# Performance work log

Hardware: AMD Instinct MI355X
Metric: run time of the kernel (lower is better)

## Reference

```python
import jax, jax.numpy as jnp
import numpy as np

H, P, N, D, T, MLPW, B = 64, 4, 16, 8, 64, 512, 2048
D_IN = 1 + H + P * H  # 321


def _linear_init(key, i, o):
    k1, k2 = jax.random.split(key)
    s = 1.0 / np.sqrt(i)
    W = jax.random.uniform(k1, (i, o), jnp.float32, -s, s)
    b = jax.random.uniform(k2, (o,), jnp.float32, -s, s)
    return W, b


def setup_inputs() -> dict:
    key = jax.random.key(0)
    ks = jax.random.split(key, 10)
    dims_f = [(D_IN, MLPW), (MLPW, MLPW), (MLPW, MLPW), (MLPW, H)]
    dims_g = [(D_IN, MLPW), (MLPW, MLPW), (MLPW, MLPW), (MLPW, H * N)]
    inp = {}
    for idx, (i, o) in enumerate(dims_f):
        W, b = _linear_init(ks[idx], i, o)
        inp[f"fW{idx}"], inp[f"fb{idx}"] = W, b
    for idx, (i, o) in enumerate(dims_g):
        W, b = _linear_init(ks[4 + idx], i, o)
        inp[f"gW{idx}"], inp[f"gb{idx}"] = W, b
    inp["rW"], inp["rb"] = _linear_init(ks[8], H, D)
    inp["ts"] = jnp.arange(T, dtype=jnp.float32)  # uniform grid, dt = 1
    inp["dbt"] = jax.random.normal(ks[9], (T - 1, B, N), jnp.float32)  # per-step randn noise
    inp["batch_size"] = B
    return inp


def _mlp(x, params):
    # Linear+ReLU stack, final Linear with tanh (tscale=1.0)
    for W, b in params[:-1]:
        x = jax.nn.relu(x @ W + b)
    W, b = params[-1]
    return jnp.tanh(x @ W + b)


def _forward(ts, dbt, fp, gp, rW, rb, batch_size):
    x0 = jnp.ones((batch_size, H), jnp.float32)  # fixed=True initial state
    dt = ts[1] - ts[0]  # dt_scale = 1
    hist = jnp.zeros((T, batch_size, H), jnp.float32).at[0].set(x0)
    curr_x, curr_t = x0, ts[0]
    xs = [x0]
    for k in range(T - 1):  # one integration step per output interval (uniform ts)
        # ortho rfft over the growing state history (length k+1); keep first P coeffs,
        # real part (matches torch complex -> .float() cast), zero-pad to P.
        coeffs = jnp.fft.rfft(hist[: k + 1], axis=0, norm="ortho")  # (F, B, H) complex
        c = jnp.real(coeffs[:P]).astype(jnp.float32)
        if c.shape[0] < P:
            c = jnp.concatenate(
                [c, jnp.zeros((P - c.shape[0], batch_size, H), jnp.float32)], axis=0
            )
        feats = jnp.transpose(c, (1, 0, 2)).reshape(batch_size, P * H)  # (B, P*H)
        tcol = jnp.broadcast_to(jnp.reshape(curr_t, (1, 1)), (batch_size, 1))
        tx = jnp.concatenate([tcol, curr_x, feats], axis=1)  # (B, 1+H+P*H)
        drift = _mlp(tx, fp)  # (B, H)
        diff = _mlp(tx, gp).reshape(batch_size, H, N)  # (B, H, N)
        curr_x = curr_x + drift * dt + jnp.einsum("bhn,bn->bh", diff, dbt[k])
        curr_t = jnp.minimum(curr_t + dt, ts[-1])
        hist = hist.at[k + 1].set(curr_x)
        xs.append(curr_x)  # linear_interp degenerates to curr_x on uniform grid
    xs = jnp.stack(xs, axis=1)  # (B, T, H)
    ys = xs @ rW + rb  # readout, (B, T, D)
    tse = jnp.broadcast_to(ts[None, :, None], (batch_size, T, 1))
    # linear_interpolation_coeffs is identity for NaN-free data
    return jnp.concatenate([tse, ys], axis=2)  # (B, T, 1+D)


def reference(fW0, fb0, fW1, fb1, fW2, fb2, fW3, fb3,
              gW0, gb0, gW1, gb1, gW2, gb2, gW3, gb3,
              rW, rb, ts, dbt, batch_size):
    fp = [(fW0, fb0), (fW1, fb1), (fW2, fb2), (fW3, fb3)]
    gp = [(gW0, gb0), (gW1, gb1), (gW2, gb2), (gW3, gb3)]
    return _forward(ts, dbt, fp, gp, rW, rb, batch_size)
```

## Files before the change

kernel.cpp:

```cpp
#include <hip/hip_runtime.h>
#include <math.h>

constexpr int kH   = 64;
constexpr int kP   = 4;
constexpr int kN   = 16;
constexpr int kD   = 8;
constexpr int kT   = 64;
constexpr int kWd  = 512;
constexpr int kB   = 2048;
constexpr int kDIN = 1 + kH + kP * kH;
constexpr int kKP  = 384;
constexpr int kBH  = kB * kH;

typedef __attribute__((ext_vector_type(8))) short short8;
typedef __attribute__((ext_vector_type(4))) float f32x4;

__device__ __forceinline__ short f2bf(float x) {
    union { float f; unsigned u; } v; v.f = x;
    unsigned r = (v.u + 0x7FFFu + ((v.u >> 16) & 1u)) >> 16;
    return (short)r;
}
__device__ __forceinline__ float bf2f(short h) {
    union { unsigned u; float f; } v; v.u = ((unsigned)(unsigned short)h) << 16;
    return v.f;
}

__device__ __forceinline__ void gload16(const short* g, short* l) {
    __builtin_amdgcn_global_load_lds(
        (const __attribute__((address_space(1))) unsigned int*)g,
        (__attribute__((address_space(3))) unsigned int*)l, 16, 0, 0);
}

__global__ __launch_bounds__(256) void transpose_bf16(const float* __restrict__ W,
                                                      short* __restrict__ Wt,
                                                      int K, int N, int Kp, int Np) {
    int idx = blockIdx.x * 256 + threadIdx.x;
    if (idx >= Kp * Np) return;
    int n = idx / Kp, kk = idx % Kp;
    float v = (kk < K && n < N) ? W[(size_t)kk * N + n] : 0.f;
    Wt[idx] = f2bf(v);
}

__global__ __launch_bounds__(256) void prep_bias(const float* __restrict__ fb0,
                                                 const float* __restrict__ gb0,
                                                 float* __restrict__ b0c) {
    int i = blockIdx.x * 256 + threadIdx.x;
    if (i < 1024) b0c[i] = (i < kWd) ? fb0[i] : gb0[i - kWd];
}

__global__ __launch_bounds__(256) void init_k(float* __restrict__ hist,
                                              short* __restrict__ txh) {
    int idx = blockIdx.x * 256 + threadIdx.x;
    if (idx < kBH) hist[idx] = 1.0f;
    if (idx < kB * (kKP - kDIN)) {
        int b = idx / (kKP - kDIN), c = idx % (kKP - kDIN);
        txh[(size_t)b * kKP + kDIN + c] = 0;
    }
}

__global__ __launch_bounds__(256) void step_pre(float* __restrict__ hist,
                                                const float* __restrict__ drift,
                                                const short* __restrict__ diffb,
                                                const float* __restrict__ dbt,
                                                short* __restrict__ txh, int k) {
    const int L = k + 1;
    __shared__ float ctab[kT * kP];
    int tid = threadIdx.x;
    float invs = rsqrtf((float)L);
    for (int i = tid; i < L * kP; i += 256) {
        int j = i >> 2, p = i & 3;
        ctab[i] = cosf(6.283185307179586f * (float)(p * j) / (float)L) * invs;
    }
    __syncthreads();
    int idx = blockIdx.x * 256 + tid;
    int b = idx >> 6, h = idx & 63;
    float xk;
    if (k == 0) {
        xk = 1.0f;
    } else {
        xk = hist[(size_t)(k - 1) * kBH + idx] + drift[idx];
        const short* dr = diffb + (size_t)b * 1024 + h * kN;
        const float* wr = dbt + (size_t)(k - 1) * kB * kN + b * kN;
#pragma unroll
        for (int n = 0; n < kN; ++n) xk += bf2f(dr[n]) * wr[n];
        hist[(size_t)k * kBH + idx] = xk;
    }
    const float* hp = hist + (size_t)b * kH + h;
    float a0 = 0.f, a1 = 0.f, a2 = 0.f, a3 = 0.f;
    for (int j = 0; j < k; ++j) {
        float x = hp[(size_t)j * kBH];
        a0 += x * ctab[j * 4 + 0];
        a1 += x * ctab[j * 4 + 1];
        a2 += x * ctab[j * 4 + 2];
        a3 += x * ctab[j * 4 + 3];
    }
    a0 += xk * ctab[k * 4 + 0];
    a1 += xk * ctab[k * 4 + 1];
    a2 += xk * ctab[k * 4 + 2];
    a3 += xk * ctab[k * 4 + 3];
    if (L < 2) a1 = 0.f;
    if (L < 4) a2 = 0.f;
    if (L < 6) a3 = 0.f;
    short* th = txh + (size_t)b * kKP;
    th[1 + kH + 0 * kH + h] = f2bf(a0);
    th[1 + kH + 1 * kH + h] = f2bf(a1);
    th[1 + kH + 2 * kH + h] = f2bf(a2);
    th[1 + kH + 3 * kH + h] = f2bf(a3);
    th[1 + h] = f2bf(xk);
    if (h == 0) th[0] = f2bf((float)k);
}

struct MArg {
    const short* A;
    const short* Bt;
    const float* bias;
    short* Cb;
    float* Cf;
    int K, lda, ldc, act, Nw;
};

__global__ __launch_bounds__(256, 2) void gemm_mfma(MArg f, MArg g, int ysplit) {
    const int y = blockIdx.y;
    MArg a;
    int n0;
    if (y < ysplit) { a = f; n0 = y * 64; }
    else            { a = g; n0 = (y - ysplit) * 64; }
    const int m0 = blockIdx.x * 64;

    __shared__ __align__(16) short sA[2][2][64 * 32];
    __shared__ __align__(16) short sB[2][2][64 * 32];

    const int tid = threadIdx.x;
    const int lane = tid & 63;
    const int w = tid >> 6;
    const int wm = (w & 1) * 32;
    const int wn = (w >> 1) * 32;

    const int sr = tid >> 2;
    const int s  = tid & 3;
    const int scol = (s ^ ((sr >> 1) & 3)) * 8;
    const int sdst = sr * 32 + s * 8;

    const short* gA = a.A  + (size_t)(m0 + sr) * a.lda + scol;
    const short* gB = a.Bt + (size_t)(n0 + sr) * a.K   + scol;

    const int nk = a.K >> 6;
    f32x4 acc[2][2] = {};

    gload16(gA,      &sA[0][0][sdst]);
    gload16(gA + 32, &sA[0][1][sdst]);
    gload16(gB,      &sB[0][0][sdst]);
    gload16(gB + 32, &sB[0][1][sdst]);

    const int fr = lane & 15;
    const int kb = ((lane >> 4) ^ ((fr >> 1) & 3)) * 8;
    const int ra0 = (wm + fr) * 32 + kb, ra1 = (wm + 16 + fr) * 32 + kb;
    const int rb0 = (wn + fr) * 32 + kb, rb1 = (wn + 16 + fr) * 32 + kb;

    for (int kt = 0; kt < nk; ++kt) {
        __syncthreads();
        const int cur = kt & 1, nxt = cur ^ 1;
        if (kt + 1 < nk) {
            const int ko = (kt + 1) << 6;
            gload16(gA + ko,      &sA[nxt][0][sdst]);
            gload16(gA + ko + 32, &sA[nxt][1][sdst]);
            gload16(gB + ko,      &sB[nxt][0][sdst]);
            gload16(gB + ko + 32, &sB[nxt][1][sdst]);
        }
#pragma unroll
        for (int ks = 0; ks < 2; ++ks) {
            short8 a0 = *(const short8*)&sA[cur][ks][ra0];
            short8 a1 = *(const short8*)&sA[cur][ks][ra1];
            short8 b0 = *(const short8*)&sB[cur][ks][rb0];
            short8 b1 = *(const short8*)&sB[cur][ks][rb1];
            acc[0][0] = __builtin_amdgcn_mfma_f32_16x16x32_bf16(a0, b0, acc[0][0], 0, 0, 0);
            acc[0][1] = __builtin_amdgcn_mfma_f32_16x16x32_bf16(a0, b1, acc[0][1], 0, 0, 0);
            acc[1][0] = __builtin_amdgcn_mfma_f32_16x16x32_bf16(a1, b0, acc[1][0], 0, 0, 0);
            acc[1][1] = __builtin_amdgcn_mfma_f32_16x16x32_bf16(a1, b1, acc[1][1], 0, 0, 0);
        }
    }

    const int rq = (lane >> 4) * 4;
#pragma unroll
    for (int j = 0; j < 2; ++j) {
        int n = n0 + wn + j * 16 + fr;
        if (n >= a.Nw) continue;
        float bias = a.bias[n];
#pragma unroll
        for (int i = 0; i < 2; ++i) {
#pragma unroll
            for (int r = 0; r < 4; ++r) {
                int m = m0 + wm + i * 16 + rq + r;
                float v = acc[i][j][r] + bias;
                if (a.act == 0) {
                    a.Cb[(size_t)m * a.ldc + n] = f2bf(fmaxf(v, 0.f));
                } else if (a.Cb) {
                    a.Cb[(size_t)m * a.ldc + n] = f2bf(tanhf(v));
                } else {
                    a.Cf[(size_t)m * a.ldc + n] = tanhf(v);
                }
            }
        }
    }
}

__global__ __launch_bounds__(256) void update_k(float* __restrict__ hist,
                                                const float* __restrict__ drift,
                                                const short* __restrict__ diffb,
                                                const float* __restrict__ dbt, int k) {
    int idx = blockIdx.x * 256 + threadIdx.x;
    int b = idx >> 6, h = idx & 63;
    float s = hist[(size_t)k * kBH + idx] + drift[idx];
    const short* dr = diffb + (size_t)b * 1024 + h * kN;
    const float* wr = dbt + (size_t)k * kB * kN + b * kN;
#pragma unroll
    for (int n = 0; n < kN; ++n) s += bf2f(dr[n]) * wr[n];
    hist[(size_t)(k + 1) * kBH + idx] = s;
}

__global__ __launch_bounds__(256) void readout_k(const float* __restrict__ hist,
                                                 const float* __restrict__ rW,
                                                 const float* __restrict__ rb,
                                                 const float* __restrict__ ts,
                                                 float* __restrict__ out) {
    __shared__ float sW[kH * kD];
    __shared__ float sb[kD];
    __shared__ float sts[kT];
    int tid = threadIdx.x;
    sW[tid] = rW[tid];
    sW[tid + 256] = rW[tid + 256];
    if (tid < kD) sb[tid] = rb[tid];
    if (tid < kT) sts[tid] = ts[tid];
    __syncthreads();
    int idx = blockIdx.x * 256 + tid;
    int t = idx & (kT - 1), b = idx >> 6;
    const float* xr = hist + (size_t)t * kBH + (size_t)b * kH;
    float acc[kD];
#pragma unroll
    for (int d = 0; d < kD; ++d) acc[d] = sb[d];
    for (int h = 0; h < kH; ++h) {
        float x = xr[h];
#pragma unroll
        for (int d = 0; d < kD; ++d) acc[d] += x * sW[h * kD + d];
    }
    float* o = out + (size_t)((size_t)b * kT + t) * (1 + kD);
    o[0] = sts[t];
#pragma unroll
    for (int d = 0; d < kD; ++d) o[1 + d] = acc[d];
}

extern "C" void kernel_launch(void* const* d_in, const int* in_sizes, int n_in,
                              void* d_out, int out_size, void* d_ws, size_t ws_size,
                              hipStream_t stream) {
    const float* fW0 = (const float*)d_in[0];  const float* fb0 = (const float*)d_in[1];
    const float* fW1 = (const float*)d_in[2];  const float* fb1 = (const float*)d_in[3];
    const float* fW2 = (const float*)d_in[4];  const float* fb2 = (const float*)d_in[5];
    const float* fW3 = (const float*)d_in[6];  const float* fb3 = (const float*)d_in[7];
    const float* gW0 = (const float*)d_in[8];  const float* gb0 = (const float*)d_in[9];
    const float* gW1 = (const float*)d_in[10]; const float* gb1 = (const float*)d_in[11];
    const float* gW2 = (const float*)d_in[12]; const float* gb2 = (const float*)d_in[13];
    const float* gW3 = (const float*)d_in[14]; const float* gb3 = (const float*)d_in[15];
    const float* rW  = (const float*)d_in[16]; const float* rb  = (const float*)d_in[17];
    const float* ts  = (const float*)d_in[18]; const float* dbt = (const float*)d_in[19];
    float* out = (float*)d_out;

    char* p = (char*)d_ws;
    float* hist  = (float*)p;  p += (size_t)kT * kBH * 4;
    float* drift = (float*)p;  p += (size_t)kBH * 4;
    float* b0c   = (float*)p;  p += 1024 * 4;
    short* diffb = (short*)p;  p += (size_t)kB * 1024 * 2;
    short* txh   = (short*)p;  p += (size_t)kB * kKP * 2;
    short* b1h   = (short*)p;  p += (size_t)kB * 1024 * 2;
    short* b2h   = (short*)p;  p += (size_t)kB * 1024 * 2;
    short* W0t   = (short*)p;  p += (size_t)1024 * kKP * 2;
    short* fW1t  = (short*)p;  p += (size_t)512 * 512 * 2;
    short* gW1t  = (short*)p;  p += (size_t)512 * 512 * 2;
    short* fW2t  = (short*)p;  p += (size_t)512 * 512 * 2;
    short* gW2t  = (short*)p;  p += (size_t)512 * 512 * 2;
    short* fW3t  = (short*)p;  p += (size_t)64 * 512 * 2;
    short* gW3t  = (short*)p;  p += (size_t)1024 * 512 * 2;

    auto tgrid = [](int n) { return dim3((n + 255) / 256); };
    transpose_bf16<<<tgrid(kKP * 512), 256, 0, stream>>>(fW0, W0t, kDIN, 512, kKP, 512);
    transpose_bf16<<<tgrid(kKP * 512), 256, 0, stream>>>(gW0, W0t + (size_t)512 * kKP, kDIN, 512, kKP, 512);
    transpose_bf16<<<tgrid(512 * 512), 256, 0, stream>>>(fW1, fW1t, 512, 512, 512, 512);
    transpose_bf16<<<tgrid(512 * 512), 256, 0, stream>>>(gW1, gW1t, 512, 512, 512, 512);
    transpose_bf16<<<tgrid(512 * 512), 256, 0, stream>>>(fW2, fW2t, 512, 512, 512, 512);
    transpose_bf16<<<tgrid(512 * 512), 256, 0, stream>>>(gW2, gW2t, 512, 512, 512, 512);
    transpose_bf16<<<tgrid(512 * 64), 256, 0, stream>>>(fW3, fW3t, 512, 64, 512, 64);
    transpose_bf16<<<tgrid(512 * 1024), 256, 0, stream>>>(gW3, gW3t, 512, 1024, 512, 1024);
    prep_bias<<<dim3(4), 256, 0, stream>>>(fb0, gb0, b0c);
    init_k<<<dim3(kBH / 256), 256, 0, stream>>>(hist, txh);

    for (int k = 0; k < kT - 1; ++k) {
        step_pre<<<dim3(kBH / 256), 256, 0, stream>>>(hist, drift, diffb, dbt, txh, k);

        MArg l1{txh, W0t, b0c, b1h, nullptr, kKP, kKP, 1024, 0, 1024};
        gemm_mfma<<<dim3(32, 16), 256, 0, stream>>>(l1, l1, 16);

        MArg f2{b1h, fW1t, fb1, b2h, nullptr, 512, 1024, 1024, 0, 512};
        MArg g2{b1h + 512, gW1t, gb1, b2h + 512, nullptr, 512, 1024, 1024, 0, 512};
        gemm_mfma<<<dim3(32, 16), 256, 0, stream>>>(f2, g2, 8);

        MArg f3{b2h, fW2t, fb2, b1h, nullptr, 512, 1024, 1024, 0, 512};
        MArg g3{b2h + 512, gW2t, gb2, b1h + 512, nullptr, 512, 1024, 1024, 0, 512};
        gemm_mfma<<<dim3(32, 16), 256, 0, stream>>>(f3, g3, 8);

        MArg f4{b1h, fW3t, fb3, nullptr, drift, 512, 1024, kH, 1, kH};
        MArg g4{b1h + 512, gW3t, gb3, diffb, nullptr, 512, 1024, 1024, 1, 1024};
        gemm_mfma<<<dim3(32, 17), 256, 0, stream>>>(f4, g4, 1);
    }

    update_k<<<dim3(kBH / 256), 256, 0, stream>>>(hist, drift, diffb, dbt, kT - 2);
    readout_k<<<dim3(kB * kT / 256), 256, 0, stream>>>(hist, rW, rb, ts, out);
}
```

Measured before the change: 2.548 ms.

## Fuse diffusion-noise contraction into last GEMM and enlarge GEMM tiles to 128 rows

The last MLP layer moves into a dedicated kernel. It applies tanh, multiplies the diffusion output by the Brownian increments staged in shared memory, and reduces over N with lane shuffles. It writes a per-(b,h) xdelta instead of a bf16 diffusion matrix, which removes the 2048x1024 intermediate write and reread and drops the bf16 rounding of diff. The general GEMM tiles grow from 64x64 with 256 threads to 128x64 with 512 threads, halving the block count and reusing each B tile across more rows. The larger tiles give fewer blocks (256) on a large-CU GPU, which may reduce occupancy.

Measured after the change: 2.608 ms. 2.4% more time.

```diff
diff --git a/kernel.cpp b/kernel.cpp
--- a/kernel.cpp
+++ b/kernel.cpp
@@ -14,15 +14,12 @@
 
 typedef __attribute__((ext_vector_type(8))) short short8;
 typedef __attribute__((ext_vector_type(4))) float f32x4;
+typedef __attribute__((ext_vector_type(4))) float float4v;
 
 __device__ __forceinline__ short f2bf(float x) {
     union { float f; unsigned u; } v; v.f = x;
     unsigned r = (v.u + 0x7FFFu + ((v.u >> 16) & 1u)) >> 16;
     return (short)r;
-}
-__device__ __forceinline__ float bf2f(short h) {
-    union { unsigned u; float f; } v; v.u = ((unsigned)(unsigned short)h) << 16;
-    return v.f;
 }
 
 __device__ __forceinline__ void gload16(const short* g, short* l) {
@@ -60,8 +57,7 @@
 
 __global__ __launch_bounds__(256) void step_pre(float* __restrict__ hist,
                                                 const float* __restrict__ drift,
-                                                const short* __restrict__ diffb,
-                                                const float* __restrict__ dbt,
+                                                const float* __restrict__ xdelta,
                                                 short* __restrict__ txh, int k) {
     const int L = k + 1;
     __shared__ float ctab[kT * kP];
@@ -78,11 +74,7 @@
     if (k == 0) {
         xk = 1.0f;
     } else {
-        xk = hist[(size_t)(k - 1) * kBH + idx] + drift[idx];
-        const short* dr = diffb + (size_t)b * 1024 + h * kN;
-        const float* wr = dbt + (size_t)(k - 1) * kB * kN + b * kN;
-#pragma unroll
-        for (int n = 0; n < kN; ++n) xk += bf2f(dr[n]) * wr[n];
+        xk = hist[(size_t)(k - 1) * kBH + idx] + drift[idx] + xdelta[idx];
         hist[(size_t)k * kBH + idx] = xk;
     }
     const float* hp = hist + (size_t)b * kH + h;
@@ -115,31 +107,31 @@
     const short* Bt;
     const float* bias;
     short* Cb;
-    float* Cf;
-    int K, lda, ldc, act, Nw;
+    int K, lda, ldc, Nw;
 };
 
-__global__ __launch_bounds__(256, 2) void gemm_mfma(MArg f, MArg g, int ysplit) {
+__global__ __launch_bounds__(512, 1) void gemm128(MArg f, MArg g, int ysplit) {
     const int y = blockIdx.y;
     MArg a;
     int n0;
     if (y < ysplit) { a = f; n0 = y * 64; }
     else            { a = g; n0 = (y - ysplit) * 64; }
-    const int m0 = blockIdx.x * 64;
-
-    __shared__ __align__(16) short sA[2][2][64 * 32];
+    const int m0 = blockIdx.x * 128;
+
+    __shared__ __align__(16) short sA[2][2][128 * 32];
     __shared__ __align__(16) short sB[2][2][64 * 32];
 
     const int tid = threadIdx.x;
     const int lane = tid & 63;
     const int w = tid >> 6;
-    const int wm = (w & 1) * 32;
-    const int wn = (w >> 1) * 32;
+    const int wm = (w & 3) * 32;
+    const int wn = (w >> 2) * 32;
 
     const int sr = tid >> 2;
     const int s  = tid & 3;
     const int scol = (s ^ ((sr >> 1) & 3)) * 8;
     const int sdst = sr * 32 + s * 8;
+    const bool doB = tid < 256;
 
     const short* gA = a.A  + (size_t)(m0 + sr) * a.lda + scol;
     const short* gB = a.Bt + (size_t)(n0 + sr) * a.K   + scol;
@@ -149,8 +141,10 @@
 
     gload16(gA,      &sA[0][0][sdst]);
     gload16(gA + 32, &sA[0][1][sdst]);
-    gload16(gB,      &sB[0][0][sdst]);
-    gload16(gB + 32, &sB[0][1][sdst]);
+    if (doB) {
+        gload16(gB,      &sB[0][0][sdst]);
+        gload16(gB + 32, &sB[0][1][sdst]);
+    }
 
     const int fr = lane & 15;
     const int kb = ((lane >> 4) ^ ((fr >> 1) & 3)) * 8;
@@ -164,8 +158,10 @@
             const int ko = (kt + 1) << 6;
             gload16(gA + ko,      &sA[nxt][0][sdst]);
             gload16(gA + ko + 32, &sA[nxt][1][sdst]);
-            gload16(gB + ko,      &sB[nxt][0][sdst]);
-            gload16(gB + ko + 32, &sB[nxt][1][sdst]);
+            if (doB) {
+                gload16(gB + ko,      &sB[nxt][0][sdst]);
+                gload16(gB + ko + 32, &sB[nxt][1][sdst]);
+            }
         }
 #pragma unroll
         for (int ks = 0; ks < 2; ++ks) {
@@ -182,40 +178,144 @@
 
     const int rq = (lane >> 4) * 4;
 #pragma unroll
-    for (int j = 0; j < 2; ++j) {
-        int n = n0 + wn + j * 16 + fr;
+    for (int jj = 0; jj < 2; ++jj) {
+        int n = n0 + wn + jj * 16 + fr;
         if (n >= a.Nw) continue;
-        float bias = a.bias[n];
-#pragma unroll
-        for (int i = 0; i < 2; ++i) {
+        float bv = a.bias[n];
+#pragma unroll
+        for (int i = 0; i < 2; ++i)
 #pragma unroll
             for (int r = 0; r < 4; ++r) {
                 int m = m0 + wm + i * 16 + rq + r;
-                float v = acc[i][j][r] + bias;
-                if (a.act == 0) {
-                    a.Cb[(size_t)m * a.ldc + n] = f2bf(fmaxf(v, 0.f));
-                } else if (a.Cb) {
-                    a.Cb[(size_t)m * a.ldc + n] = f2bf(tanhf(v));
-                } else {
-                    a.Cf[(size_t)m * a.ldc + n] = tanhf(v);
+                a.Cb[(size_t)m * a.ldc + n] = f2bf(fmaxf(acc[i][jj][r] + bv, 0.f));
+            }
+    }
+}
+
+__global__ __launch_bounds__(512, 1) void l4_kernel(const short* __restrict__ b1,
+                                                    const short* __restrict__ fW3t,
+                                                    const float* __restrict__ fb3,
+                                                    const short* __restrict__ gW3t,
+                                                    const float* __restrict__ gb3,
+                                                    const float* __restrict__ dbt,
+                                                    float* __restrict__ drift,
+                                                    float* __restrict__ xdelta, int k) {
+    const int y = blockIdx.y;
+    const bool isF = (y == 0);
+    const int nt = isF ? 0 : y - 1;
+    const int n0 = nt * 64;
+    const int m0 = blockIdx.x * 128;
+
+    __shared__ __align__(16) short sA[2][2][128 * 32];
+    __shared__ __align__(16) short sB[2][2][64 * 32];
+    __shared__ float sdb[128 * 16];
+
+    const int tid = threadIdx.x;
+    const int lane = tid & 63;
+    const int w = tid >> 6;
+    const int wm = (w & 3) * 32;
+    const int wn = (w >> 2) * 32;
+
+    const short* A = b1 + (isF ? 0 : 512);
+    const short* Bt = isF ? fW3t : gW3t + (size_t)n0 * 512;
+    const float* bias = isF ? fb3 : gb3 + n0;
+    const int K = 512;
+
+    if (!isF)
+        *(float4v*)&sdb[tid * 4] =
+            ((const float4v*)(dbt + ((size_t)k * kB + m0) * kN))[tid];
+
+    const int sr = tid >> 2;
+    const int s  = tid & 3;
+    const int scol = (s ^ ((sr >> 1) & 3)) * 8;
+    const int sdst = sr * 32 + s * 8;
+    const bool doB = tid < 256;
+
+    const short* gA = A + (size_t)(m0 + sr) * 1024 + scol;
+    const short* gB = Bt + (size_t)sr * K + scol;
+
+    f32x4 acc[2][2] = {};
+    gload16(gA,      &sA[0][0][sdst]);
+    gload16(gA + 32, &sA[0][1][sdst]);
+    if (doB) {
+        gload16(gB,      &sB[0][0][sdst]);
+        gload16(gB + 32, &sB[0][1][sdst]);
+    }
+
+    const int fr = lane & 15;
+    const int kb = ((lane >> 4) ^ ((fr >> 1) & 3)) * 8;
+    const int ra0 = (wm + fr) * 32 + kb, ra1 = (wm + 16 + fr) * 32 + kb;
+    const int rb0 = (wn + fr) * 32 + kb, rb1 = (wn + 16 + fr) * 32 + kb;
+
+    for (int kt = 0; kt < 8; ++kt) {
+        __syncthreads();
+        const int cur = kt & 1, nxt = cur ^ 1;
+        if (kt + 1 < 8) {
+            const int ko = (kt + 1) << 6;
+            gload16(gA + ko,      &sA[nxt][0][sdst]);
+            gload16(gA + ko + 32, &sA[nxt][1][sdst]);
+            if (doB) {
+                gload16(gB + ko,      &sB[nxt][0][sdst]);
+                gload16(gB + ko + 32, &sB[nxt][1][sdst]);
+            }
+        }
+#pragma unroll
+        for (int ks = 0; ks < 2; ++ks) {
+            short8 a0 = *(const short8*)&sA[cur][ks][ra0];
+            short8 a1 = *(const short8*)&sA[cur][ks][ra1];
+            short8 b0 = *(const short8*)&sB[cur][ks][rb0];
+            short8 b1 = *(const short8*)&sB[cur][ks][rb1];
+            acc[0][0] = __builtin_amdgcn_mfma_f32_16x16x32_bf16(a0, b0, acc[0][0], 0, 0, 0);
+            acc[0][1] = __builtin_amdgcn_mfma_f32_16x16x32_bf16(a0, b1, acc[0][1], 0, 0, 0);
+            acc[1][0] = __builtin_amdgcn_mfma_f32_16x16x32_bf16(a1, b0, acc[1][0], 0, 0, 0);
+            acc[1][1] = __builtin_amdgcn_mfma_f32_16x16x32_bf16(a1, b1, acc[1][1], 0, 0, 0);
+        }
+    }
+
+    const int rq = (lane >> 4) * 4;
+    if (isF) {
+#pragma unroll
+        for (int jj = 0; jj < 2; ++jj) {
+            int n = wn + jj * 16 + fr;
+            float bv = bias[n];
+#pragma unroll
+            for (int i = 0; i < 2; ++i)
+#pragma unroll
+                for (int r = 0; r < 4; ++r) {
+                    int m = m0 + wm + i * 16 + rq + r;
+                    drift[(size_t)m * kH + n] = tanhf(acc[i][jj][r] + bv);
                 }
-            }
+        }
+    } else {
+#pragma unroll
+        for (int jj = 0; jj < 2; ++jj) {
+            int n = wn + jj * 16 + fr;
+            float bv = bias[n];
+            int h = (n0 + wn + jj * 16) >> 4;
+#pragma unroll
+            for (int i = 0; i < 2; ++i)
+#pragma unroll
+                for (int r = 0; r < 4; ++r) {
+                    int mr = wm + i * 16 + rq + r;
+                    float v = tanhf(acc[i][jj][r] + bv);
+                    float p = v * sdb[mr * 16 + fr];
+                    p += __shfl_xor(p, 1);
+                    p += __shfl_xor(p, 2);
+                    p += __shfl_xor(p, 4);
+                    p += __shfl_xor(p, 8);
+                    if (fr == 0)
+                        xdelta[(size_t)(m0 + mr) * kH + h] = p;
+                }
         }
     }
 }
 
 __global__ __launch_bounds__(256) void update_k(float* __restrict__ hist,
                                                 const float* __restrict__ drift,
-                                                const short* __restrict__ diffb,
-                                                const float* __restrict__ dbt, int k) {
+                                                const float* __restrict__ xdelta, int k) {
     int idx = blockIdx.x * 256 + threadIdx.x;
-    int b = idx >> 6, h = idx & 63;
-    float s = hist[(size_t)k * kBH + idx] + drift[idx];
-    const short* dr = diffb + (size_t)b * 1024 + h * kN;
-    const float* wr = dbt + (size_t)k * kB * kN + b * kN;
-#pragma unroll
-    for (int n = 0; n < kN; ++n) s += bf2f(dr[n]) * wr[n];
-    hist[(size_t)(k + 1) * kBH + idx] = s;
+    hist[(size_t)(k + 1) * kBH + idx] =
+        hist[(size_t)k * kBH + idx] + drift[idx] + xdelta[idx];
 }
 
 __global__ __launch_bounds__(256) void readout_k(const float* __restrict__ hist,
@@ -265,20 +365,20 @@
     float* out = (float*)d_out;
 
     char* p = (char*)d_ws;
-    float* hist  = (float*)p;  p += (size_t)kT * kBH * 4;
-    float* drift = (float*)p;  p += (size_t)kBH * 4;
-    float* b0c   = (float*)p;  p += 1024 * 4;
-    short* diffb = (short*)p;  p += (size_t)kB * 1024 * 2;
-    short* txh   = (short*)p;  p += (size_t)kB * kKP * 2;
-    short* b1h   = (short*)p;  p += (size_t)kB * 1024 * 2;
-    short* b2h   = (short*)p;  p += (size_t)kB * 1024 * 2;
-    short* W0t   = (short*)p;  p += (size_t)1024 * kKP * 2;
-    short* fW1t  = (short*)p;  p += (size_t)512 * 512 * 2;
-    short* gW1t  = (short*)p;  p += (size_t)512 * 512 * 2;
-    short* fW2t  = (short*)p;  p += (size_t)512 * 512 * 2;
-    short* gW2t  = (short*)p;  p += (size_t)512 * 512 * 2;
-    short* fW3t  = (short*)p;  p += (size_t)64 * 512 * 2;
-    short* gW3t  = (short*)p;  p += (size_t)1024 * 512 * 2;
+    float* hist   = (float*)p;  p += (size_t)kT * kBH * 4;
+    float* drift  = (float*)p;  p += (size_t)kBH * 4;
+    float* xdelta = (float*)p;  p += (size_t)kBH * 4;
+    float* b0c    = (float*)p;  p += 1024 * 4;
+    short* txh    = (short*)p;  p += (size_t)kB * kKP * 2;
+    short* b1h    = (short*)p;  p += (size_t)kB * 1024 * 2;
+    short* b2h    = (short*)p;  p += (size_t)kB * 1024 * 2;
+    short* W0t    = (short*)p;  p += (size_t)1024 * kKP * 2;
+    short* fW1t   = (short*)p;  p += (size_t)512 * 512 * 2;
+    short* gW1t   = (short*)p;  p += (size_t)512 * 512 * 2;
+    short* fW2t   = (short*)p;  p += (size_t)512 * 512 * 2;
+    short* gW2t   = (short*)p;  p += (size_t)512 * 512 * 2;
+    short* fW3t   = (short*)p;  p += (size_t)64 * 512 * 2;
+    short* gW3t   = (short*)p;  p += (size_t)1024 * 512 * 2;
 
     auto tgrid = [](int n) { return dim3((n + 255) / 256); };
     transpose_bf16<<<tgrid(kKP * 512), 256, 0, stream>>>(fW0, W0t, kDIN, 512, kKP, 512);
@@ -293,24 +393,23 @@
     init_k<<<dim3(kBH / 256), 256, 0, stream>>>(hist, txh);
 
     for (int k = 0; k < kT - 1; ++k) {
-        step_pre<<<dim3(kBH / 256), 256, 0, stream>>>(hist, drift, diffb, dbt, txh, k);
-
-        MArg l1{txh, W0t, b0c, b1h, nullptr, kKP, kKP, 1024, 0, 1024};
-        gemm_mfma<<<dim3(32, 16), 256, 0, stream>>>(l1, l1, 16);
-
-        MArg f2{b1h, fW1t, fb1, b2h, nullptr, 512, 1024, 1024, 0, 512};
-        MArg g2{b1h + 512, gW1t, gb1, b2h + 512, nullptr, 512, 1024, 1024, 0, 512};
-        gemm_mfma<<<dim3(32, 16), 256, 0, stream>>>(f2, g2, 8);
-
-        MArg f3{b2h, fW2t, fb2, b1h, nullptr, 512, 1024, 1024, 0, 512};
-        MArg g3{b2h + 512, gW2t, gb2, b1h + 512, nullptr, 512, 1024, 1024, 0, 512};
-        gemm_mfma<<<dim3(32, 16), 256, 0, stream>>>(f3, g3, 8);
-
-        MArg f4{b1h, fW3t, fb3, nullptr, drift, 512, 1024, kH, 1, kH};
-        MArg g4{b1h + 512, gW3t, gb3, diffb, nullptr, 512, 1024, 1024, 1, 1024};
-        gemm_mfma<<<dim3(32, 17), 256, 0, stream>>>(f4, g4, 1);
-    }
-
-    update_k<<<dim3(kBH / 256), 256, 0, stream>>>(hist, drift, diffb, dbt, kT - 2);
+        step_pre<<<dim3(kBH / 256), 256, 0, stream>>>(hist, drift, xdelta, txh, k);
+
+        MArg l1{txh, W0t, b0c, b1h, kKP, kKP, 1024, 1024};
+        gemm128<<<dim3(16, 16), 512, 0, stream>>>(l1, l1, 16);
+
+        MArg f2{b1h, fW1t, fb1, b2h, 512, 1024, 1024, 512};
+        MArg g2{b1h + 512, gW1t, gb1, b2h + 512, 512, 1024, 1024, 512};
+        gemm128<<<dim3(16, 16), 512, 0, stream>>>(f2, g2, 8);
+
+        MArg f3{b2h, fW2t, fb2, b1h, 512, 1024, 1024, 512};
+        MArg g3{b2h + 512, gW2t, gb2, b1h + 512, 512, 1024, 1024, 512};
+        gemm128<<<dim3(16, 16), 512, 0, stream>>>(f3, g3, 8);
+
+        l4_kernel<<<dim3(16, 17), 512, 0, stream>>>(b1h, fW3t, fb3, gW3t, gb3,
+                                                    dbt, drift, xdelta, k);
+    }
+
+    update_k<<<dim3(kBH / 256), 256, 0, stream>>>(hist, drift, xdelta, kT - 2);
     readout_k<<<dim3(kB * kT / 256), 256, 0, stream>>>(hist, rW, rb, ts, out);
 }
```
